# Optimization experiments

Measured on AMD Instinct MI355X. Metric: run time of the kernel, lower is better.

The kernel has to match this reference:

```python
import jax, jax.numpy as jnp
import numpy as np

N, E, IN_F, EDGE_F, HID, S = 200000, 600000, 28, 4, 128, 20000
NUM_LAYERS = 4
L = NUM_LAYERS - 1
BN_EPS = 1e-5


def setup_inputs() -> dict:
    key = jax.random.key(0)
    ks = jax.random.split(key, 20)
    p = lambda k, shape: (jax.random.normal(k, shape, dtype=jnp.float32) * 0.1)
    return {
        'x': jax.random.normal(ks[0], (N, IN_F), dtype=jnp.float32),
        'edge_index': jax.random.randint(ks[1], (2, E), 0, N),
        'edge_attr': jax.random.normal(ks[2], (E, EDGE_F), dtype=jnp.float32),
        'edge_weight': jax.random.uniform(ks[3], (E,), dtype=jnp.float32),
        'node_mask': (jax.random.uniform(ks[4], (N,)) > 0.5).astype(jnp.float32),
        'subgraphs2nodes': jax.random.randint(ks[5], (N,), 0, S),
        # layer-1 params (in_features -> hidden)
        'be1_W1': p(ks[6], (EDGE_F, IN_F)), 'be1_b1': jnp.zeros((IN_F,), jnp.float32),
        'be1_W2': p(ks[7], (IN_F, IN_F)), 'be1_b2': jnp.zeros((IN_F,), jnp.float32),
        'm1_W1': p(ks[8], (IN_F, HID)), 'm1_b1': jnp.zeros((HID,), jnp.float32),
        'm1_W2': p(ks[9], (HID, HID)), 'm1_b2': jnp.zeros((HID,), jnp.float32),
        'bn1_g': jnp.ones((HID,), jnp.float32), 'bn1_b': jnp.zeros((HID,), jnp.float32),
        'eps1': jnp.zeros((), jnp.float32),
        # layers 2..NUM_LAYERS, stacked (hidden -> hidden)
        'beW1': p(ks[10], (L, EDGE_F, HID)), 'beb1': jnp.zeros((L, HID), jnp.float32),
        'beW2': p(ks[11], (L, HID, HID)), 'beb2': jnp.zeros((L, HID), jnp.float32),
        'mW1': p(ks[12], (L, HID, HID)), 'mb1': jnp.zeros((L, HID), jnp.float32),
        'mW2': p(ks[13], (L, HID, HID)), 'mb2': jnp.zeros((L, HID), jnp.float32),
        'bng': jnp.ones((L, HID), jnp.float32), 'bnb': jnp.zeros((L, HID), jnp.float32),
        'eps': jnp.zeros((L,), jnp.float32),
    }


def _mlp2(h, W1, b1, W2, b2):
    # Linear -> ReLU -> Linear
    return jnp.dot(jax.nn.relu(jnp.dot(h, W1) + b1), W2) + b2


def _gine(x, src, dst, edge_attr, edge_weight, eps,
          beW1, beb1, beW2, beb2, W1, b1, W2, b2, g, beta):
    # bond encoder on edge features
    e = _mlp2(edge_attr, beW1, beb1, beW2, beb2)            # [E, d]
    # message: relu(x_j + e_ij) * w_ij, aggregated at dst via scatter-add
    m = jax.nn.relu(x[src] + e) * edge_weight[:, None]      # [E, d]
    aggr = jax.ops.segment_sum(m, dst, num_segments=N)      # [N, d]
    h = (1.0 + eps) * x + aggr
    # node MLP: Linear,ReLU,Linear,BN(train mode),ReLU
    h = _mlp2(h, W1, b1, W2, b2)
    mu = jnp.mean(h, axis=0)
    var = jnp.mean((h - mu) ** 2, axis=0)
    h = (h - mu) * jax.lax.rsqrt(var + BN_EPS) * g + beta
    return jax.nn.relu(h)


def reference(x, edge_index, edge_attr, edge_weight, node_mask, subgraphs2nodes,
              be1_W1, be1_b1, be1_W2, be1_b2, m1_W1, m1_b1, m1_W2, m1_b2,
              bn1_g, bn1_b, eps1,
              beW1, beb1, beW2, beb2, mW1, mb1, mW2, mb2, bng, bnb, eps):
    src, dst = edge_index[0], edge_index[1]
    h = _gine(x, src, dst, edge_attr, edge_weight, eps1,
              be1_W1, be1_b1, be1_W2, be1_b2,
              m1_W1, m1_b1, m1_W2, m1_b2, bn1_g, bn1_b)
    for i in range(L):
        h_new = _gine(h, src, dst, edge_attr, edge_weight, eps[i],
                      beW1[i], beb1[i], beW2[i], beb2[i],
                      mW1[i], mb1[i], mW2[i], mb2[i], bng[i], bnb[i])
        h = h + h_new  # residual
    # float node_mask branch + global_add_pool over subgraphs2nodes
    h = h * node_mask[:, None]
    return jax.ops.segment_sum(h, subgraphs2nodes, num_segments=S)  # [S, HID]
```

## Files before the change

kernel.cpp:

```cpp
#include <hip/hip_runtime.h>
#include <hip/hip_bf16.h>


#define BNEPS 1e-5f
#define LDA 136
#define SCAN_NB 240

typedef __attribute__((ext_vector_type(8))) short bf16x8;
typedef __attribute__((ext_vector_type(8))) unsigned short u16x8;
typedef __attribute__((ext_vector_type(4))) float f32x4;

__device__ inline short f2bf(float f) {
    __hip_bfloat16 h = __float2bfloat16(f);
    return *reinterpret_cast<short*>(&h);
}
__device__ inline unsigned short f2bfu(float f) {
    __hip_bfloat16 h = __float2bfloat16(f);
    return *reinterpret_cast<unsigned short*>(&h);
}
__device__ inline float bf2f(unsigned short u) {
    union { unsigned int i; float f; } v; v.i = ((unsigned int)u) << 16; return v.f;
}


__global__ __launch_bounds__(256) void k_prep(
    const float* __restrict__ m1W2, const float* __restrict__ beW2,
    const float* __restrict__ mW1, const float* __restrict__ mW2,
    const float* __restrict__ m1W1, const float* __restrict__ be1W2,
    short* __restrict__ out, short* __restrict__ out1, short* __restrict__ out28)
{
    __shared__ float tileS[64][65];
    int b = blockIdx.x;
    if (b == 40) {
        for (int i = threadIdx.x; i < 4096; i += 256) {
            int j = i & 7, sub = (i >> 3) & 63, nt = i >> 9;
            int quad = sub >> 4, l15 = sub & 15;
            int n = nt * 16 + l15, k = quad * 8 + j;
            out1[i] = (k < 28) ? f2bf(m1W1[(size_t)k * 128 + n]) : (short)0;
        }
        return;
    }
    if (b == 41) {
        for (int i = threadIdx.x; i < 1024; i += 256) {
            int j = i & 7, lane = (i >> 3) & 63, nt = i >> 9;
            int quad = lane >> 4, l15 = lane & 15;
            int n = nt * 16 + l15, k = quad * 8 + j;
            out28[i] = (n < 28 && k < 28) ? f2bf(be1W2[(size_t)k * 28 + n]) : (short)0;
        }
        return;
    }
    int mat = b >> 2, t = b & 3;
    const float* Wsrc;
    if (mat == 0) Wsrc = m1W2;
    else {
        int l = (mat - 1) / 3, which = (mat - 1) % 3;
        Wsrc = (which == 0) ? beW2 + (size_t)l * 16384
             : (which == 1) ? mW1 + (size_t)l * 16384
             :                mW2 + (size_t)l * 16384;
    }
    short* dst = out + (size_t)mat * 16384;
    int tr = (t >> 1) * 64, tc = (t & 1) * 64;
    for (int i = threadIdx.x; i < 4096; i += 256) {
        int r = i >> 6, c = i & 63;
        tileS[r][c] = Wsrc[(size_t)(tr + r) * 128 + (tc + c)];
    }
    __syncthreads();
    for (int i = threadIdx.x; i < 4096; i += 256) {
        int kl = i & 63, nl = i >> 6;
        int n = tc + nl, k = tr + kl;
        int fo = (((n >> 4) * 4 + (k >> 5)) * 64 + (((k >> 3) & 3) * 16 + (n & 15))) * 8 + (k & 7);
        dst[fo] = f2bf(tileS[kl][nl]);
    }
}

__global__ __launch_bounds__(256) void k_prepx(
    const float* __restrict__ x, unsigned short* __restrict__ xbf, int N)
{
    int total = N * 32;
    for (int i = blockIdx.x * 256 + threadIdx.x; i < total; i += gridDim.x * 256) {
        int n = i >> 5, c = i & 31;
        xbf[i] = (c < 28) ? f2bfu(x[(size_t)n * 28 + c]) : (unsigned short)0;
    }
}

__global__ __launch_bounds__(256) void k_count(
    const int* __restrict__ ei, int* __restrict__ counts, int E)
{
    for (int e = blockIdx.x * 256 + threadIdx.x; e < E; e += gridDim.x * 256)
        atomicAdd(&counts[ei[E + e]], 1);
}

__global__ __launch_bounds__(256) void k_count2(
    const int* __restrict__ s2n, const float* __restrict__ mask,
    int* __restrict__ counts2, int N)
{
    for (int n = blockIdx.x * 256 + threadIdx.x; n < N; n += gridDim.x * 256)
        if (mask[n] != 0.f) atomicAdd(&counts2[s2n[n]], 1);
}

__global__ __launch_bounds__(256) void k_scanA(
    const int* __restrict__ counts, int* __restrict__ bsum, int N, int seg)
{
    __shared__ int red[256];
    int b = blockIdx.x;
    int lo = b * seg, hi = min(lo + seg, N);
    int s = 0;
    for (int i = lo + threadIdx.x; i < hi; i += 256) s += counts[i];
    red[threadIdx.x] = s;
    __syncthreads();
    for (int d = 128; d > 0; d >>= 1) {
        if (threadIdx.x < d) red[threadIdx.x] += red[threadIdx.x + d];
        __syncthreads();
    }
    if (threadIdx.x == 0) bsum[b] = red[0];
}

__global__ __launch_bounds__(256) void k_scanB(
    int* __restrict__ bsum, int nb, int* __restrict__ offs, int N)
{
    __shared__ int sh[256];
    int v = (threadIdx.x < nb) ? bsum[threadIdx.x] : 0;
    sh[threadIdx.x] = v;
    __syncthreads();
    for (int d = 1; d < 256; d <<= 1) {
        int t = (threadIdx.x >= d) ? sh[threadIdx.x - d] : 0;
        __syncthreads();
        sh[threadIdx.x] += t;
        __syncthreads();
    }
    if (threadIdx.x < nb) bsum[threadIdx.x] = sh[threadIdx.x] - v;
    if (threadIdx.x == 0) offs[N] = sh[255];
}

__global__ __launch_bounds__(256) void k_scanC(
    const int* __restrict__ counts, const int* __restrict__ bsum,
    int* __restrict__ offs, int* __restrict__ cursor, int N, int seg)
{
    __shared__ int sh[256];
    int b = blockIdx.x;
    int lo = b * seg, hi = min(lo + seg, N);
    int base = bsum[b];
    for (int t0 = lo; t0 < hi; t0 += 256) {
        int i = t0 + threadIdx.x;
        int v = (i < hi) ? counts[i] : 0;
        sh[threadIdx.x] = v;
        __syncthreads();
        for (int d = 1; d < 256; d <<= 1) {
            int t = (threadIdx.x >= d) ? sh[threadIdx.x - d] : 0;
            __syncthreads();
            sh[threadIdx.x] += t;
            __syncthreads();
        }
        int excl = base + sh[threadIdx.x] - v;
        if (i < hi) { offs[i] = excl; cursor[i] = excl; }
        int tileTotal = sh[255];
        __syncthreads();
        base += tileTotal;
    }
}

__global__ __launch_bounds__(256) void k_scatter(
    const int* __restrict__ ei, const float* __restrict__ ew,
    const float4* __restrict__ ea4,
    int* __restrict__ cursor, int2* __restrict__ pmeta,
    float4* __restrict__ pea4, int E)
{
    for (int e = blockIdx.x * 256 + threadIdx.x; e < E; e += gridDim.x * 256) {
        int d = ei[E + e];
        int pos = atomicAdd(&cursor[d], 1);
        pmeta[pos] = make_int2(ei[e], __float_as_int(ew[e]));
        pea4[pos] = ea4[e];
    }
}

__global__ __launch_bounds__(256) void k_scatter2(
    const int* __restrict__ s2n, const float* __restrict__ mask,
    int* __restrict__ cursor2, int* __restrict__ perm2, int N)
{
    for (int n = blockIdx.x * 256 + threadIdx.x; n < N; n += gridDim.x * 256)
        if (mask[n] != 0.f) {
            int pos = atomicAdd(&cursor2[s2n[n]], 1);
            perm2[pos] = n;
        }
}

__global__ __launch_bounds__(256, 3) void k_emsg(
    const float4* __restrict__ pea4,
    const float* __restrict__ W1, const float* __restrict__ b1,
    const short* __restrict__ W2f, const float* __restrict__ b2,
    unsigned short* __restrict__ emsg, const int* __restrict__ offs,
    int n0, int n1)
{
    __shared__ short As[64 * LDA];
    __shared__ short Bs[16384];
    int e0 = offs[n0], e1 = offs[n1];
    int tid = threadIdx.x;
    int w = tid >> 6, lane = tid & 63;
    int l15 = lane & 15, quad = lane >> 4;
    int rb = w * 16;
    for (int i = tid; i < 2048; i += 256)
        *(bf16x8*)&Bs[i * 8] = *(const bf16x8*)&W2f[i * 8];
    int c2 = lane * 2;
    float w1a[4], w1b[4];
    #pragma unroll
    for (int a = 0; a < 4; ++a) { w1a[a] = W1[a * 128 + c2]; w1b[a] = W1[a * 128 + c2 + 1]; }
    float b1a = b1[c2], b1b = b1[c2 + 1];
    float b2r[8];
    #pragma unroll
    for (int nt = 0; nt < 8; ++nt) b2r[nt] = b2[nt * 16 + l15];
    __syncthreads();

    const float* peaf = (const float*)pea4;
    int numTiles = (e1 - e0 + 63) >> 6;
    for (int tile = blockIdx.x; tile < numTiles; tile += gridDim.x) {
        int base = e0 + tile * 64;
        int eidx = base + rb + (lane >> 2);
        float v = (eidx < e1) ? peaf[(size_t)(base + rb) * 4 + lane] : 0.f;
        #pragma unroll
        for (int e = 0; e < 16; ++e) {
            float a0v = __shfl(v, e * 4 + 0);
            float a1v = __shfl(v, e * 4 + 1);
            float a2v = __shfl(v, e * 4 + 2);
            float a3v = __shfl(v, e * 4 + 3);
            float t0 = fmaf(a0v, w1a[0], fmaf(a1v, w1a[1], fmaf(a2v, w1a[2], fmaf(a3v, w1a[3], b1a))));
            float t1 = fmaf(a0v, w1b[0], fmaf(a1v, w1b[1], fmaf(a2v, w1b[2], fmaf(a3v, w1b[3], b1b))));
            unsigned int pk = ((unsigned int)f2bfu(fmaxf(t1, 0.f)) << 16) | f2bfu(fmaxf(t0, 0.f));
            *(unsigned int*)&As[(rb + e) * LDA + c2] = pk;
        }
        f32x4 acc[8];
        #pragma unroll
        for (int nt = 0; nt < 8; ++nt) acc[nt] = (f32x4){0.f, 0.f, 0.f, 0.f};
        #pragma unroll
        for (int kt = 0; kt < 4; ++kt) {
            bf16x8 af = *(bf16x8*)&As[(rb + l15) * LDA + kt * 32 + quad * 8];
            #pragma unroll
            for (int nt = 0; nt < 8; ++nt) {
                bf16x8 bf = *(const bf16x8*)&Bs[((nt * 4 + kt) * 64 + lane) * 8];
                acc[nt] = __builtin_amdgcn_mfma_f32_16x16x32_bf16(af, bf, acc[nt], 0, 0, 0);
            }
        }
        #pragma unroll
        for (int nt = 0; nt < 8; ++nt) {
            #pragma unroll
            for (int r = 0; r < 4; ++r)
                As[(rb + quad * 4 + r) * LDA + nt * 16 + l15] = f2bf(acc[nt][r] + b2r[nt]);
        }
        #pragma unroll
        for (int it = 0; it < 4; ++it) {
            int arow = rb + it * 4 + quad;
            int gr = base + arow;
            if (gr < e1)
                *(bf16x8*)&emsg[(size_t)(gr - e0) * 128 + l15 * 8] = *(bf16x8*)&As[arow * LDA + l15 * 8];
        }
    }
}

__global__ __launch_bounds__(256, 4) void k_emsg28_mm(
    const float4* __restrict__ pea4,
    const float* __restrict__ W1, const float* __restrict__ b1,
    const short* __restrict__ W2f28,
    const float* __restrict__ b2,
    unsigned short* __restrict__ emsg28, int E)
{
    __shared__ short As[64 * 40];
    int tid = threadIdx.x;
    int w = tid >> 6, lane = tid & 63;
    int l15 = lane & 15, quad = lane >> 4;
    int rb = w * 16;
    bf16x8 B0 = *(const bf16x8*)&W2f28[(size_t)lane * 8];
    bf16x8 B1 = *(const bf16x8*)&W2f28[(size_t)(64 + lane) * 8];
    int c2 = l15 * 2;
    bool act = (c2 < 28);
    float w1a[4], w1b[4], b1a, b1b;
    #pragma unroll
    for (int a = 0; a < 4; ++a) {
        w1a[a] = act ? W1[a * 28 + c2] : 0.f;
        w1b[a] = act ? W1[a * 28 + c2 + 1] : 0.f;
    }
    b1a = act ? b1[c2] : 0.f;
    b1b = act ? b1[c2 + 1] : 0.f;
    float b2r0 = b2[l15];
    float b2r1 = (l15 < 12) ? b2[16 + l15] : 0.f;

    const float* peaf = (const float*)pea4;
    int numTiles = (E + 63) >> 6;
    for (int tile = blockIdx.x; tile < numTiles; tile += gridDim.x) {
        int base = tile * 64;
        int eidx = base + rb + (lane >> 2);
        float v = (eidx < E) ? peaf[(size_t)(base + rb) * 4 + lane] : 0.f;
        #pragma unroll
        for (int e = 0; e < 16; ++e) {
            float a0v = __shfl(v, e * 4 + 0);
            float a1v = __shfl(v, e * 4 + 1);
            float a2v = __shfl(v, e * 4 + 2);
            float a3v = __shfl(v, e * 4 + 3);
            float t0 = fmaf(a0v, w1a[0], fmaf(a1v, w1a[1], fmaf(a2v, w1a[2], fmaf(a3v, w1a[3], b1a))));
            float t1 = fmaf(a0v, w1b[0], fmaf(a1v, w1b[1], fmaf(a2v, w1b[2], fmaf(a3v, w1b[3], b1b))));
            unsigned int pk = ((unsigned int)f2bfu(fmaxf(t1, 0.f)) << 16) | f2bfu(fmaxf(t0, 0.f));
            if (quad == (e & 3))
                *(unsigned int*)&As[(rb + e) * 40 + c2] = pk;
        }
        f32x4 acc0 = (f32x4){0.f, 0.f, 0.f, 0.f};
        f32x4 acc1 = (f32x4){0.f, 0.f, 0.f, 0.f};
        bf16x8 af = *(bf16x8*)&As[(rb + l15) * 40 + quad * 8];
        acc0 = __builtin_amdgcn_mfma_f32_16x16x32_bf16(af, B0, acc0, 0, 0, 0);
        acc1 = __builtin_amdgcn_mfma_f32_16x16x32_bf16(af, B1, acc1, 0, 0, 0);
        #pragma unroll
        for (int r = 0; r < 4; ++r) {
            As[(rb + quad * 4 + r) * 40 + l15] = f2bf(acc0[r] + b2r0);
            As[(rb + quad * 4 + r) * 40 + 16 + l15] = f2bf(acc1[r] + b2r1);
        }
        #pragma unroll
        for (int it = 0; it < 4; ++it) {
            int arow = rb + it * 4 + quad;
            int gr = base + arow;
            if (gr < E && l15 < 14)
                *(ushort2*)&emsg28[(size_t)gr * 28 + c2] = *(ushort2*)&As[arow * 40 + c2];
        }
    }
}

__global__ __launch_bounds__(256) void k_gather(
    const unsigned short* __restrict__ h, const int* __restrict__ offs,
    const int2* __restrict__ pmeta, const unsigned short* __restrict__ emsg,
    unsigned short* __restrict__ a0,
    const float* __restrict__ epsp, int epsIdx,
    int n0, int n1)
{
    int grp = threadIdx.x >> 5, lane = threadIdx.x & 31;
    int n = n0 + blockIdx.x * 8 + grp;
    if (n >= n1) return;
    int e0 = offs[n0];
    int k0 = offs[n], k1 = offs[n + 1];
    float s = 1.0f + epsp[epsIdx];
    ushort4 hv0 = *(const ushort4*)&h[(size_t)n * 128 + lane * 4];
    float m0 = s * bf2f(hv0.x), m1 = s * bf2f(hv0.y);
    float m2 = s * bf2f(hv0.z), m3 = s * bf2f(hv0.w);
    int2 mtA, mtB;
    ushort4 evA, hvA, evB, hvB;
    if (k0 < k1) {
        mtA = pmeta[k0];
        evA = *(const ushort4*)&emsg[(size_t)(k0 - e0) * 128 + lane * 4];
        hvA = *(const ushort4*)&h[(size_t)mtA.x * 128 + lane * 4];
    }
    if (k0 + 1 < k1) {
        mtB = pmeta[k0 + 1];
        evB = *(const ushort4*)&emsg[(size_t)(k0 + 1 - e0) * 128 + lane * 4];
        hvB = *(const ushort4*)&h[(size_t)mtB.x * 128 + lane * 4];
    }
    for (int k = k0; k < k1; ++k) {
        float w = __int_as_float(mtA.y);
        m0 += fmaxf(bf2f(hvA.x) + bf2f(evA.x), 0.f) * w;
        m1 += fmaxf(bf2f(hvA.y) + bf2f(evA.y), 0.f) * w;
        m2 += fmaxf(bf2f(hvA.z) + bf2f(evA.z), 0.f) * w;
        m3 += fmaxf(bf2f(hvA.w) + bf2f(evA.w), 0.f) * w;
        mtA = mtB; evA = evB; hvA = hvB;
        if (k + 2 < k1) {
            mtB = pmeta[k + 2];
            evB = *(const ushort4*)&emsg[(size_t)(k + 2 - e0) * 128 + lane * 4];
            hvB = *(const ushort4*)&h[(size_t)mtB.x * 128 + lane * 4];
        }
    }
    ushort4 o;
    o.x = f2bfu(m0); o.y = f2bfu(m1); o.z = f2bfu(m2); o.w = f2bfu(m3);
    *(ushort4*)&a0[(size_t)n * 128 + lane * 4] = o;
}

__global__ __launch_bounds__(256) void k_gather28(
    const float* __restrict__ x, const unsigned short* __restrict__ xbf,
    const int* __restrict__ offs,
    const int2* __restrict__ pmeta, const unsigned short* __restrict__ emsg28,
    const float* __restrict__ eps1, float* __restrict__ u28, int N)
{
    int grp = threadIdx.x >> 5, lane = threadIdx.x & 31;
    int n = blockIdx.x * 8 + grp;
    if (n >= N || lane >= 28) return;
    float s = 1.0f + eps1[0];
    int k0 = offs[n], k1 = offs[n + 1];
    float m = 0.f;
    int2 mtA, mtB;
    unsigned short eA = 0, xA = 0, eB = 0, xB = 0;
    if (k0 < k1) {
        mtA = pmeta[k0];
        eA = emsg28[(size_t)k0 * 28 + lane];
        xA = xbf[(size_t)mtA.x * 32 + lane];
    }
    if (k0 + 1 < k1) {
        mtB = pmeta[k0 + 1];
        eB = emsg28[(size_t)(k0 + 1) * 28 + lane];
        xB = xbf[(size_t)mtB.x * 32 + lane];
    }
    for (int k = k0; k < k1; ++k) {
        float w = __int_as_float(mtA.y);
        m += fmaxf(bf2f(xA) + bf2f(eA), 0.f) * w;
        mtA = mtB; eA = eB; xA = xB;
        if (k + 2 < k1) {
            mtB = pmeta[k + 2];
            eB = emsg28[(size_t)(k + 2) * 28 + lane];
            xB = xbf[(size_t)mtB.x * 32 + lane];
        }
    }
    u28[(size_t)n * 28 + lane] = fmaf(s, x[(size_t)n * 28 + lane], m);
}

__global__ __launch_bounds__(512, 2) void k_mlp(
    const unsigned short* __restrict__ src, const short* __restrict__ W1f,
    const float* __restrict__ b1, const short* __restrict__ W2f,
    const float* __restrict__ b2, unsigned short* __restrict__ dst,
    float* __restrict__ stats, int N)
{
    __shared__ short As[256 * LDA];
    __shared__ short Bs1[16384];
    __shared__ short Bs2[16384];
    __shared__ float sstat[256];
    int tid = threadIdx.x;
    for (int i = tid; i < 2048; i += 512) {
        *(bf16x8*)&Bs1[i * 8] = *(const bf16x8*)&W1f[i * 8];
        *(bf16x8*)&Bs2[i * 8] = *(const bf16x8*)&W2f[i * 8];
    }
    if (tid < 256) sstat[tid] = 0.f;
    int w = tid >> 6, lane = tid & 63;
    int l15 = lane & 15, quad = lane >> 4;
    int rb = w * 32;
    float b1r[8], b2r[8], lsum[8], lsq[8];
    #pragma unroll
    for (int nt = 0; nt < 8; ++nt) {
        b1r[nt] = b1[nt * 16 + l15]; b2r[nt] = b2[nt * 16 + l15];
        lsum[nt] = 0.f; lsq[nt] = 0.f;
    }
    int numTiles = (N + 255) >> 8;
    bf16x8 st[8];
    {
        int tile = blockIdx.x;
        if (tile < numTiles) {
            int base = tile * 256;
            #pragma unroll
            for (int kk = 0; kk < 8; ++kk) {
                int i = tid + kk * 512;
                int rr = base + (i >> 4);
                st[kk] = (rr < N) ? *(const bf16x8*)&src[(size_t)rr * 128 + (i & 15) * 8]
                                  : (bf16x8){0, 0, 0, 0, 0, 0, 0, 0};
            }
        }
    }
    __syncthreads();

    for (int tile = blockIdx.x; tile < numTiles; tile += gridDim.x) {
        int base = tile * 256;
        #pragma unroll
        for (int kk = 0; kk < 8; ++kk) {
            int i = tid + kk * 512;
            *(bf16x8*)&As[(i >> 4) * LDA + (i & 15) * 8] = st[kk];
        }
        int tnext = tile + gridDim.x;
        if (tnext < numTiles) {
            int bn = tnext * 256;
            #pragma unroll
            for (int kk = 0; kk < 8; ++kk) {
                int i = tid + kk * 512;
                int rr = bn + (i >> 4);
                st[kk] = (rr < N) ? *(const bf16x8*)&src[(size_t)rr * 128 + (i & 15) * 8]
                                  : (bf16x8){0, 0, 0, 0, 0, 0, 0, 0};
            }
        }
        __syncthreads();
        f32x4 acc[2][8];
        #pragma unroll
        for (int rg = 0; rg < 2; ++rg)
            #pragma unroll
            for (int nt = 0; nt < 8; ++nt) acc[rg][nt] = (f32x4){0.f, 0.f, 0.f, 0.f};
        #pragma unroll
        for (int kt = 0; kt < 4; ++kt) {
            bf16x8 af0 = *(bf16x8*)&As[(rb + l15) * LDA + kt * 32 + quad * 8];
            bf16x8 af1 = *(bf16x8*)&As[(rb + 16 + l15) * LDA + kt * 32 + quad * 8];
            #pragma unroll
            for (int nt = 0; nt < 8; ++nt) {
                bf16x8 bf = *(const bf16x8*)&Bs1[((nt * 4 + kt) * 64 + lane) * 8];
                acc[0][nt] = __builtin_amdgcn_mfma_f32_16x16x32_bf16(af0, bf, acc[0][nt], 0, 0, 0);
                acc[1][nt] = __builtin_amdgcn_mfma_f32_16x16x32_bf16(af1, bf, acc[1][nt], 0, 0, 0);
            }
        }
        #pragma unroll
        for (int rg = 0; rg < 2; ++rg)
            #pragma unroll
            for (int nt = 0; nt < 8; ++nt)
                #pragma unroll
                for (int r = 0; r < 4; ++r)
                    As[(rb + rg * 16 + quad * 4 + r) * LDA + nt * 16 + l15] =
                        f2bf(fmaxf(acc[rg][nt][r] + b1r[nt], 0.f));
        #pragma unroll
        for (int rg = 0; rg < 2; ++rg)
            #pragma unroll
            for (int nt = 0; nt < 8; ++nt) acc[rg][nt] = (f32x4){0.f, 0.f, 0.f, 0.f};
        #pragma unroll
        for (int kt = 0; kt < 4; ++kt) {
            bf16x8 af0 = *(bf16x8*)&As[(rb + l15) * LDA + kt * 32 + quad * 8];
            bf16x8 af1 = *(bf16x8*)&As[(rb + 16 + l15) * LDA + kt * 32 + quad * 8];
            #pragma unroll
            for (int nt = 0; nt < 8; ++nt) {
                bf16x8 bf = *(const bf16x8*)&Bs2[((nt * 4 + kt) * 64 + lane) * 8];
                acc[0][nt] = __builtin_amdgcn_mfma_f32_16x16x32_bf16(af0, bf, acc[0][nt], 0, 0, 0);
                acc[1][nt] = __builtin_amdgcn_mfma_f32_16x16x32_bf16(af1, bf, acc[1][nt], 0, 0, 0);
            }
        }
        #pragma unroll
        for (int rg = 0; rg < 2; ++rg)
            #pragma unroll
            for (int nt = 0; nt < 8; ++nt) {
                int row0 = base + rb + rg * 16 + quad * 4;
                #pragma unroll
                for (int r = 0; r < 4; ++r) {
                    float z = acc[rg][nt][r] + b2r[nt];
                    if (row0 + r < N) { lsum[nt] += z; lsq[nt] = fmaf(z, z, lsq[nt]); }
                    As[(rb + rg * 16 + quad * 4 + r) * LDA + nt * 16 + l15] = f2bf(z);
                }
            }
        #pragma unroll
        for (int it = 0; it < 8; ++it) {
            int arow = rb + it * 4 + quad;
            int rr = base + arow;
            if (rr < N)
                *(bf16x8*)&dst[(size_t)rr * 128 + l15 * 8] = *(bf16x8*)&As[arow * LDA + l15 * 8];
        }
        __syncthreads();
    }
    #pragma unroll
    for (int nt = 0; nt < 8; ++nt) {
        atomicAdd(&sstat[nt * 16 + l15], lsum[nt]);
        atomicAdd(&sstat[128 + nt * 16 + l15], lsq[nt]);
    }
    __syncthreads();
    if (tid < 256) atomicAdd(&stats[tid], sstat[tid]);
}

__global__ __launch_bounds__(512, 2) void k_mlp1(
    const float* __restrict__ u28, const short* __restrict__ W1f,
    const float* __restrict__ b1, const short* __restrict__ W2f,
    const float* __restrict__ b2, unsigned short* __restrict__ dst,
    float* __restrict__ stats, int N)
{
    __shared__ short A28[256 * 40];
    __shared__ short As[256 * LDA];
    __shared__ short Bs1[4096];
    __shared__ short Bs2[16384];
    __shared__ float sstat[256];
    int tid = threadIdx.x;
    if (tid < 512) {
        int i = tid;
        *(bf16x8*)&Bs1[i * 8] = *(const bf16x8*)&W1f[i * 8];
    }
    for (int i = tid; i < 2048; i += 512)
        *(bf16x8*)&Bs2[i * 8] = *(const bf16x8*)&W2f[i * 8];
    for (int i = tid; i < 1024; i += 512) {
        int row = i >> 2, c = 28 + (i & 3);
        A28[row * 40 + c] = 0;
    }
    if (tid < 256) sstat[tid] = 0.f;
    int w = tid >> 6, lane = tid & 63;
    int l15 = lane & 15, quad = lane >> 4;
    int rb = w * 32;
    float b1r[8], b2r[8], lsum[8], lsq[8];
    #pragma unroll
    for (int nt = 0; nt < 8; ++nt) {
        b1r[nt] = b1[nt * 16 + l15]; b2r[nt] = b2[nt * 16 + l15];
        lsum[nt] = 0.f; lsq[nt] = 0.f;
    }
    int numTiles = (N + 255) >> 8;
    float stf[14];
    {
        int tile = blockIdx.x;
        if (tile < numTiles) {
            int base = tile * 256;
            #pragma unroll
            for (int kk = 0; kk < 14; ++kk) {
                int idx = tid + kk * 512;
                int row = idx / 28, col = idx - row * 28;
                int rr = base + row;
                stf[kk] = (rr < N) ? u28[(size_t)rr * 28 + col] : 0.f;
            }
        }
    }
    __syncthreads();

    for (int tile = blockIdx.x; tile < numTiles; tile += gridDim.x) {
        int base = tile * 256;
        #pragma unroll
        for (int kk = 0; kk < 14; ++kk) {
            int idx = tid + kk * 512;
            int row = idx / 28, col = idx - row * 28;
            A28[row * 40 + col] = f2bf(stf[kk]);
        }
        int tnext = tile + gridDim.x;
        if (tnext < numTiles) {
            int bn = tnext * 256;
            #pragma unroll
            for (int kk = 0; kk < 14; ++kk) {
                int idx = tid + kk * 512;
                int row = idx / 28, col = idx - row * 28;
                int rr = bn + row;
                stf[kk] = (rr < N) ? u28[(size_t)rr * 28 + col] : 0.f;
            }
        }
        __syncthreads();
        f32x4 acc[2][8];
        #pragma unroll
        for (int rg = 0; rg < 2; ++rg)
            #pragma unroll
            for (int nt = 0; nt < 8; ++nt) acc[rg][nt] = (f32x4){0.f, 0.f, 0.f, 0.f};
        {
            bf16x8 af0 = *(bf16x8*)&A28[(rb + l15) * 40 + quad * 8];
            bf16x8 af1 = *(bf16x8*)&A28[(rb + 16 + l15) * 40 + quad * 8];
            #pragma unroll
            for (int nt = 0; nt < 8; ++nt) {
                bf16x8 bf = *(const bf16x8*)&Bs1[(nt * 64 + lane) * 8];
                acc[0][nt] = __builtin_amdgcn_mfma_f32_16x16x32_bf16(af0, bf, acc[0][nt], 0, 0, 0);
                acc[1][nt] = __builtin_amdgcn_mfma_f32_16x16x32_bf16(af1, bf, acc[1][nt], 0, 0, 0);
            }
        }
        #pragma unroll
        for (int rg = 0; rg < 2; ++rg)
            #pragma unroll
            for (int nt = 0; nt < 8; ++nt)
                #pragma unroll
                for (int r = 0; r < 4; ++r)
                    As[(rb + rg * 16 + quad * 4 + r) * LDA + nt * 16 + l15] =
                        f2bf(fmaxf(acc[rg][nt][r] + b1r[nt], 0.f));
        #pragma unroll
        for (int rg = 0; rg < 2; ++rg)
            #pragma unroll
            for (int nt = 0; nt < 8; ++nt) acc[rg][nt] = (f32x4){0.f, 0.f, 0.f, 0.f};
        #pragma unroll
        for (int kt = 0; kt < 4; ++kt) {
            bf16x8 af0 = *(bf16x8*)&As[(rb + l15) * LDA + kt * 32 + quad * 8];
            bf16x8 af1 = *(bf16x8*)&As[(rb + 16 + l15) * LDA + kt * 32 + quad * 8];
            #pragma unroll
            for (int nt = 0; nt < 8; ++nt) {
                bf16x8 bf = *(const bf16x8*)&Bs2[((nt * 4 + kt) * 64 + lane) * 8];
                acc[0][nt] = __builtin_amdgcn_mfma_f32_16x16x32_bf16(af0, bf, acc[0][nt], 0, 0, 0);
                acc[1][nt] = __builtin_amdgcn_mfma_f32_16x16x32_bf16(af1, bf, acc[1][nt], 0, 0, 0);
            }
        }
        #pragma unroll
        for (int rg = 0; rg < 2; ++rg)
            #pragma unroll
            for (int nt = 0; nt < 8; ++nt) {
                int row0 = base + rb + rg * 16 + quad * 4;
                #pragma unroll
                for (int r = 0; r < 4; ++r) {
                    float z = acc[rg][nt][r] + b2r[nt];
                    if (row0 + r < N) { lsum[nt] += z; lsq[nt] = fmaf(z, z, lsq[nt]); }
                    As[(rb + rg * 16 + quad * 4 + r) * LDA + nt * 16 + l15] = f2bf(z);
                }
            }
        #pragma unroll
        for (int it = 0; it < 8; ++it) {
            int arow = rb + it * 4 + quad;
            int rr = base + arow;
            if (rr < N)
                *(bf16x8*)&dst[(size_t)rr * 128 + l15 * 8] = *(bf16x8*)&As[arow * LDA + l15 * 8];
        }
        __syncthreads();
    }
    #pragma unroll
    for (int nt = 0; nt < 8; ++nt) {
        atomicAdd(&sstat[nt * 16 + l15], lsum[nt]);
        atomicAdd(&sstat[128 + nt * 16 + l15], lsq[nt]);
    }
    __syncthreads();
    if (tid < 256) atomicAdd(&stats[tid], sstat[tid]);
}

__global__ __launch_bounds__(128) void k_stats(
    const float* __restrict__ stats, const float* __restrict__ g,
    const float* __restrict__ b, float* __restrict__ ss, float invN)
{
    int j = threadIdx.x;
    float mu  = stats[j] * invN;
    float var = fmaf(stats[128 + j], invN, -mu * mu);
    float sc  = rsqrtf(fmaxf(var, 0.f) + BNEPS) * g[j];
    ss[j] = sc;
    ss[128 + j] = fmaf(-mu, sc, b[j]);
}

__global__ __launch_bounds__(256) void k_bn(
    const unsigned short* __restrict__ z, const float* __restrict__ ss,
    unsigned short* __restrict__ h, int residual, int N)
{
    int idx8 = blockIdx.x * 256 + threadIdx.x;
    int stride = gridDim.x * 256;
    int c0 = (idx8 & 15) * 8;
    float scl[8], sht[8];
    #pragma unroll
    for (int r = 0; r < 8; ++r) { scl[r] = ss[c0 + r]; sht[r] = ss[128 + c0 + r]; }
    int total8 = N * 16;
    for (; idx8 < total8; idx8 += stride) {
        int n = idx8 >> 4;
        u16x8 z8 = *(const u16x8*)&z[(size_t)n * 128 + c0];
        float hn[8];
        #pragma unroll
        for (int r = 0; r < 8; ++r)
            hn[r] = fmaxf(fmaf(bf2f(z8[r]), scl[r], sht[r]), 0.f);
        if (residual) {
            u16x8 h8 = *(const u16x8*)&h[(size_t)n * 128 + c0];
            #pragma unroll
            for (int r = 0; r < 8; ++r) hn[r] += bf2f(h8[r]);
        }
        u16x8 o;
        #pragma unroll
        for (int r = 0; r < 8; ++r) o[r] = f2bfu(hn[r]);
        *(u16x8*)&h[(size_t)n * 128 + c0] = o;
    }
}

__global__ __launch_bounds__(256) void k_poolbn(
    const unsigned short* __restrict__ z, const unsigned short* __restrict__ hprev,
    const float* __restrict__ ss, const int* __restrict__ offs2,
    const int* __restrict__ perm2, float* __restrict__ out, int S)
{
    int w = threadIdx.x >> 6, lane = threadIdx.x & 63;
    int s = blockIdx.x * 4 + w;
    if (s >= S) return;
    int c0 = lane * 2;
    float scl0 = ss[c0], scl1 = ss[c0 + 1];
    float sht0 = ss[128 + c0], sht1 = ss[128 + c0 + 1];
    int k0 = offs2[s], k1 = offs2[s + 1];
    float a0 = 0.f, a1 = 0.f;
    for (int k = k0; k < k1; ++k) {
        int n = perm2[k];
        ushort2 zv = *(const ushort2*)&z[(size_t)n * 128 + c0];
        ushort2 hv = *(const ushort2*)&hprev[(size_t)n * 128 + c0];
        a0 += fmaxf(fmaf(bf2f(zv.x), scl0, sht0), 0.f) + bf2f(hv.x);
        a1 += fmaxf(fmaf(bf2f(zv.y), scl1, sht1), 0.f) + bf2f(hv.y);
    }
    *(float2*)&out[(size_t)s * 128 + c0] = make_float2(a0, a1);
}

extern "C" void kernel_launch(void* const* d_in, const int* in_sizes, int n_in,
                              void* d_out, int out_size, void* d_ws, size_t ws_size,
                              hipStream_t stream) {
    const float* x    = (const float*)d_in[0];
    const int*   ei   = (const int*)d_in[1];
    const float* ea   = (const float*)d_in[2];
    const float* ew   = (const float*)d_in[3];
    const float* mask = (const float*)d_in[4];
    const int*   s2n  = (const int*)d_in[5];
    const float* be1W1 = (const float*)d_in[6];
    const float* be1b1 = (const float*)d_in[7];
    const float* be1W2 = (const float*)d_in[8];
    const float* be1b2 = (const float*)d_in[9];
    const float* m1W1  = (const float*)d_in[10];
    const float* m1b1  = (const float*)d_in[11];
    const float* m1W2  = (const float*)d_in[12];
    const float* m1b2  = (const float*)d_in[13];
    const float* bn1g  = (const float*)d_in[14];
    const float* bn1b  = (const float*)d_in[15];
    const float* eps1  = (const float*)d_in[16];
    const float* beW1  = (const float*)d_in[17];
    const float* beb1  = (const float*)d_in[18];
    const float* beW2  = (const float*)d_in[19];
    const float* beb2  = (const float*)d_in[20];
    const float* mW1   = (const float*)d_in[21];
    const float* mb1   = (const float*)d_in[22];
    const float* mW2   = (const float*)d_in[23];
    const float* mb2   = (const float*)d_in[24];
    const float* bng   = (const float*)d_in[25];
    const float* bnb   = (const float*)d_in[26];
    const float* epsL  = (const float*)d_in[27];

    const int N = in_sizes[0] / 28;
    const int E = in_sizes[1] / 2;
    const int S = out_size / 128;
    const float invN = 1.0f / (float)N;
    const int NS = N / 2;
    const int EMC = E / 2 + 8192;

    auto al16 = [](size_t v) { return (v + 15) & ~(size_t)15; };
    char* ws = (char*)d_ws;
    size_t offH      = 0;
    size_t offA0     = al16(offH + (size_t)N * 256);
    size_t offEm     = al16(offA0 + (size_t)N * 256);
    size_t emBytes   = (size_t)EMC * 256;
    if ((size_t)E * 56 > emBytes) emBytes = (size_t)E * 56;
    size_t offStats  = al16(offEm + emBytes);
    size_t offSS     = al16(offStats + 4096);
    size_t offWts    = al16(offSS + 1024);
    size_t offCounts = al16(offWts + 10 * 16384 * 2 + 4096 * 2 + 1024 * 2);
    size_t offOffs   = al16(offCounts + (size_t)N * 4);
    size_t offCursor = al16(offOffs + (size_t)(N + 1) * 4);
    size_t offPmeta  = al16(offCursor + (size_t)N * 4);
    size_t offPea    = al16(offPmeta + (size_t)E * 8);
    size_t offBsum   = al16(offPea + (size_t)E * 16);
    size_t offCnt2   = al16(offBsum + SCAN_NB * 4);
    size_t offOffs2  = al16(offCnt2 + (size_t)S * 4);
    size_t offCur2   = al16(offOffs2 + (size_t)(S + 1) * 4);
    size_t offPerm2  = al16(offCur2 + (size_t)S * 4);
    size_t need      = offPerm2 + (size_t)N * 4;
    if (ws_size < need) return;

    unsigned short* h    = (unsigned short*)(ws + offH);
    unsigned short* a0   = (unsigned short*)(ws + offA0);
    unsigned short* emsg = (unsigned short*)(ws + offEm);
    float* u28    = (float*)(ws + offA0);
    unsigned short* xbf = (unsigned short*)(ws + offA0 + 26214400);
    float* stats  = (float*)(ws + offStats);
    float* ssbuf  = (float*)(ws + offSS);
    short* wts    = (short*)(ws + offWts);
    short* w1p    = wts + 10 * 16384;
    short* w2p28  = w1p + 4096;
    int*   counts = (int*)(ws + offCounts);
    int*   offs   = (int*)(ws + offOffs);
    int*   cursor = (int*)(ws + offCursor);
    int2*  pmeta  = (int2*)(ws + offPmeta);
    float4* pea4  = (float4*)(ws + offPea);
    int*   bsum   = (int*)(ws + offBsum);
    int*   cnt2   = (int*)(ws + offCnt2);
    int*   offs2  = (int*)(ws + offOffs2);
    int*   cur2   = (int*)(ws + offCur2);
    int*   perm2  = (int*)(ws + offPerm2);
    const float4* ea4 = (const float4*)ea;

    hipMemsetAsync(stats, 0, 4 * 256 * sizeof(float), stream);
    hipMemsetAsync(counts, 0, (size_t)N * sizeof(int), stream);
    hipMemsetAsync(cnt2, 0, (size_t)S * sizeof(int), stream);

    k_prep<<<42, 256, 0, stream>>>(m1W2, beW2, mW1, mW2, m1W1, be1W2, wts, w1p, w2p28);
    k_prepx<<<512, 256, 0, stream>>>(x, xbf, N);

    const int seg = (N + SCAN_NB - 1) / SCAN_NB;
    k_count<<<1024, 256, 0, stream>>>(ei, counts, E);
    k_scanA<<<SCAN_NB, 256, 0, stream>>>(counts, bsum, N, seg);
    k_scanB<<<1, 256, 0, stream>>>(bsum, SCAN_NB, offs, N);
    k_scanC<<<SCAN_NB, 256, 0, stream>>>(counts, bsum, offs, cursor, N, seg);
    k_scatter<<<1024, 256, 0, stream>>>(ei, ew, ea4, cursor, pmeta, pea4, E);

    const int seg2 = (S + SCAN_NB - 1) / SCAN_NB;
    k_count2<<<512, 256, 0, stream>>>(s2n, mask, cnt2, N);
    k_scanA<<<SCAN_NB, 256, 0, stream>>>(cnt2, bsum, S, seg2);
    k_scanB<<<1, 256, 0, stream>>>(bsum, SCAN_NB, offs2, S);
    k_scanC<<<SCAN_NB, 256, 0, stream>>>(cnt2, bsum, offs2, cur2, S, seg2);
    k_scatter2<<<512, 256, 0, stream>>>(s2n, mask, cur2, perm2, N);

    auto wt_be = [&](int l) { return wts + (size_t)(1 + 3 * l + 0) * 16384; };
    auto wt_m1 = [&](int l) { return wts + (size_t)(1 + 3 * l + 1) * 16384; };
    auto wt_m2 = [&](int l) { return wts + (size_t)(1 + 3 * l + 2) * 16384; };

    k_emsg28_mm<<<2048, 256, 0, stream>>>(pea4, be1W1, be1b1, w2p28, be1b2, emsg, E);
    k_gather28<<<(N + 7) / 8, 256, 0, stream>>>(x, xbf, offs, pmeta, emsg, eps1, u28, N);
    k_mlp1<<<256, 512, 0, stream>>>(u28, w1p, m1b1, wts , m1b2, h, stats, N);
    k_stats<<<1, 128, 0, stream>>>(stats, bn1g, bn1b, ssbuf, invN);
    k_bn<<<2048, 256, 0, stream>>>(h, ssbuf, h, 0, N);

    for (int l = 0; l < 3; ++l) {
        for (int c = 0; c < 2; ++c) {
            int n0 = (c == 0) ? 0 : NS;
            int n1 = (c == 0) ? NS : N;
            k_emsg<<<2048, 256, 0, stream>>>(pea4,
                beW1 + (size_t)l * 512, beb1 + (size_t)l * 128,
                wt_be(l), beb2 + (size_t)l * 128, emsg, offs, n0, n1);
            k_gather<<<(n1 - n0 + 7) / 8, 256, 0, stream>>>(h, offs, pmeta, emsg, a0,
                epsL, l, n0, n1);
        }
        k_mlp<<<256, 512, 0, stream>>>(a0, wt_m1(l), mb1 + (size_t)l * 128,
                                       wt_m2(l), mb2 + (size_t)l * 128, a0,
                                       stats + 256 * (l + 1), N);
        k_stats<<<1, 128, 0, stream>>>(stats + 256 * (l + 1),
            bng + (size_t)l * 128, bnb + (size_t)l * 128, ssbuf, invN);
        if (l < 2) {
            k_bn<<<2048, 256, 0, stream>>>(a0, ssbuf, h, 1, N);
        }
    }

    k_poolbn<<<(S + 3) / 4, 256, 0, stream>>>(a0, h, ssbuf, offs2, perm2,
                                              (float*)d_out, S);
}
```

Measured before the change: 1.035 ms.

## Make MLP kernels wave-independent with direct global A loads and 1024-thread blocks

Restructures k_mlp and k_mlp1 so each wave handles its own 16-row slice. Input fragments are loaded straight from global memory into MFMA registers instead of being staged through a shared 256-row tile. Per-tile block-wide __syncthreads and the register prefetch of the next tile are removed, and blocks grow to 1024 threads to keep more waves resident. The trade-off is the loss of explicit load prefetching and a tighter register budget under launch_bounds(1024,4), which risks spilling; the A fragment loads are also less coalesced.

New measurement: 1.056 ms. 1.02x slower.

```diff
diff --git a/kernel.cpp b/kernel.cpp
--- a/kernel.cpp
+++ b/kernel.cpp
@@ -403,126 +403,86 @@
     u28[(size_t)n * 28 + lane] = fmaf(s, x[(size_t)n * 28 + lane], m);
 }
 
-__global__ __launch_bounds__(512, 2) void k_mlp(
+__global__ __launch_bounds__(1024, 4) void k_mlp(
     const unsigned short* __restrict__ src, const short* __restrict__ W1f,
     const float* __restrict__ b1, const short* __restrict__ W2f,
     const float* __restrict__ b2, unsigned short* __restrict__ dst,
     float* __restrict__ stats, int N)
 {
-    __shared__ short As[256 * LDA];
     __shared__ short Bs1[16384];
     __shared__ short Bs2[16384];
+    __shared__ short As[16 * 16 * LDA];
     __shared__ float sstat[256];
     int tid = threadIdx.x;
-    for (int i = tid; i < 2048; i += 512) {
+    for (int i = tid; i < 2048; i += 1024) {
         *(bf16x8*)&Bs1[i * 8] = *(const bf16x8*)&W1f[i * 8];
         *(bf16x8*)&Bs2[i * 8] = *(const bf16x8*)&W2f[i * 8];
     }
     if (tid < 256) sstat[tid] = 0.f;
     int w = tid >> 6, lane = tid & 63;
     int l15 = lane & 15, quad = lane >> 4;
-    int rb = w * 32;
+    short* myAs = &As[w * 16 * LDA];
     float b1r[8], b2r[8], lsum[8], lsq[8];
     #pragma unroll
     for (int nt = 0; nt < 8; ++nt) {
         b1r[nt] = b1[nt * 16 + l15]; b2r[nt] = b2[nt * 16 + l15];
         lsum[nt] = 0.f; lsq[nt] = 0.f;
     }
+    __syncthreads();
+
     int numTiles = (N + 255) >> 8;
-    bf16x8 st[8];
-    {
-        int tile = blockIdx.x;
-        if (tile < numTiles) {
-            int base = tile * 256;
-            #pragma unroll
-            for (int kk = 0; kk < 8; ++kk) {
-                int i = tid + kk * 512;
-                int rr = base + (i >> 4);
-                st[kk] = (rr < N) ? *(const bf16x8*)&src[(size_t)rr * 128 + (i & 15) * 8]
-                                  : (bf16x8){0, 0, 0, 0, 0, 0, 0, 0};
-            }
-        }
-    }
-    __syncthreads();
-
     for (int tile = blockIdx.x; tile < numTiles; tile += gridDim.x) {
-        int base = tile * 256;
-        #pragma unroll
-        for (int kk = 0; kk < 8; ++kk) {
-            int i = tid + kk * 512;
-            *(bf16x8*)&As[(i >> 4) * LDA + (i & 15) * 8] = st[kk];
-        }
-        int tnext = tile + gridDim.x;
-        if (tnext < numTiles) {
-            int bn = tnext * 256;
-            #pragma unroll
-            for (int kk = 0; kk < 8; ++kk) {
-                int i = tid + kk * 512;
-                int rr = bn + (i >> 4);
-                st[kk] = (rr < N) ? *(const bf16x8*)&src[(size_t)rr * 128 + (i & 15) * 8]
-                                  : (bf16x8){0, 0, 0, 0, 0, 0, 0, 0};
-            }
-        }
-        __syncthreads();
-        f32x4 acc[2][8];
-        #pragma unroll
-        for (int rg = 0; rg < 2; ++rg)
-            #pragma unroll
-            for (int nt = 0; nt < 8; ++nt) acc[rg][nt] = (f32x4){0.f, 0.f, 0.f, 0.f};
+        int rowbase = tile * 256 + w * 16;
+        int arow = rowbase + l15;
+        const unsigned short* srow = src + (size_t)arow * 128;
+        f32x4 acc[8];
+        #pragma unroll
+        for (int nt = 0; nt < 8; ++nt) acc[nt] = (f32x4){0.f, 0.f, 0.f, 0.f};
         #pragma unroll
         for (int kt = 0; kt < 4; ++kt) {
-            bf16x8 af0 = *(bf16x8*)&As[(rb + l15) * LDA + kt * 32 + quad * 8];
-            bf16x8 af1 = *(bf16x8*)&As[(rb + 16 + l15) * LDA + kt * 32 + quad * 8];
+            bf16x8 af = (arow < N) ? *(const bf16x8*)&srow[kt * 32 + quad * 8]
+                                   : (bf16x8){0, 0, 0, 0, 0, 0, 0, 0};
             #pragma unroll
             for (int nt = 0; nt < 8; ++nt) {
                 bf16x8 bf = *(const bf16x8*)&Bs1[((nt * 4 + kt) * 64 + lane) * 8];
-                acc[0][nt] = __builtin_amdgcn_mfma_f32_16x16x32_bf16(af0, bf, acc[0][nt], 0, 0, 0);
-                acc[1][nt] = __builtin_amdgcn_mfma_f32_16x16x32_bf16(af1, bf, acc[1][nt], 0, 0, 0);
+                acc[nt] = __builtin_amdgcn_mfma_f32_16x16x32_bf16(af, bf, acc[nt], 0, 0, 0);
             }
         }
         #pragma unroll
-        for (int rg = 0; rg < 2; ++rg)
-            #pragma unroll
-            for (int nt = 0; nt < 8; ++nt)
-                #pragma unroll
-                for (int r = 0; r < 4; ++r)
-                    As[(rb + rg * 16 + quad * 4 + r) * LDA + nt * 16 + l15] =
-                        f2bf(fmaxf(acc[rg][nt][r] + b1r[nt], 0.f));
-        #pragma unroll
-        for (int rg = 0; rg < 2; ++rg)
-            #pragma unroll
-            for (int nt = 0; nt < 8; ++nt) acc[rg][nt] = (f32x4){0.f, 0.f, 0.f, 0.f};
+        for (int nt = 0; nt < 8; ++nt)
+            #pragma unroll
+            for (int r = 0; r < 4; ++r)
+                myAs[(quad * 4 + r) * LDA + nt * 16 + l15] =
+                    f2bf(fmaxf(acc[nt][r] + b1r[nt], 0.f));
+        #pragma unroll
+        for (int nt = 0; nt < 8; ++nt) acc[nt] = (f32x4){0.f, 0.f, 0.f, 0.f};
         #pragma unroll
         for (int kt = 0; kt < 4; ++kt) {
-            bf16x8 af0 = *(bf16x8*)&As[(rb + l15) * LDA + kt * 32 + quad * 8];
-            bf16x8 af1 = *(bf16x8*)&As[(rb + 16 + l15) * LDA + kt * 32 + quad * 8];
+            bf16x8 af = *(bf16x8*)&myAs[l15 * LDA + kt * 32 + quad * 8];
             #pragma unroll
             for (int nt = 0; nt < 8; ++nt) {
                 bf16x8 bf = *(const bf16x8*)&Bs2[((nt * 4 + kt) * 64 + lane) * 8];
-                acc[0][nt] = __builtin_amdgcn_mfma_f32_16x16x32_bf16(af0, bf, acc[0][nt], 0, 0, 0);
-                acc[1][nt] = __builtin_amdgcn_mfma_f32_16x16x32_bf16(af1, bf, acc[1][nt], 0, 0, 0);
+                acc[nt] = __builtin_amdgcn_mfma_f32_16x16x32_bf16(af, bf, acc[nt], 0, 0, 0);
             }
         }
         #pragma unroll
-        for (int rg = 0; rg < 2; ++rg)
-            #pragma unroll
-            for (int nt = 0; nt < 8; ++nt) {
-                int row0 = base + rb + rg * 16 + quad * 4;
-                #pragma unroll
-                for (int r = 0; r < 4; ++r) {
-                    float z = acc[rg][nt][r] + b2r[nt];
-                    if (row0 + r < N) { lsum[nt] += z; lsq[nt] = fmaf(z, z, lsq[nt]); }
-                    As[(rb + rg * 16 + quad * 4 + r) * LDA + nt * 16 + l15] = f2bf(z);
-                }
+        for (int nt = 0; nt < 8; ++nt) {
+            int row0 = rowbase + quad * 4;
+            #pragma unroll
+            for (int r = 0; r < 4; ++r) {
+                float z = acc[nt][r] + b2r[nt];
+                if (row0 + r < N) { lsum[nt] += z; lsq[nt] = fmaf(z, z, lsq[nt]); }
+                myAs[(quad * 4 + r) * LDA + nt * 16 + l15] = f2bf(z);
             }
-        #pragma unroll
-        for (int it = 0; it < 8; ++it) {
-            int arow = rb + it * 4 + quad;
-            int rr = base + arow;
+        }
+        #pragma unroll
+        for (int s = 0; s < 4; ++s) {
+            int i = lane + s * 64;
+            int lrow = i >> 4, c8 = i & 15;
+            int rr = rowbase + lrow;
             if (rr < N)
-                *(bf16x8*)&dst[(size_t)rr * 128 + l15 * 8] = *(bf16x8*)&As[arow * LDA + l15 * 8];
-        }
-        __syncthreads();
+                *(bf16x8*)&dst[(size_t)rr * 128 + c8 * 8] = *(bf16x8*)&myAs[lrow * LDA + c8 * 8];
+        }
     }
     #pragma unroll
     for (int nt = 0; nt < 8; ++nt) {
@@ -533,133 +493,90 @@
     if (tid < 256) atomicAdd(&stats[tid], sstat[tid]);
 }
 
-__global__ __launch_bounds__(512, 2) void k_mlp1(
+__global__ __launch_bounds__(1024, 4) void k_mlp1(
     const float* __restrict__ u28, const short* __restrict__ W1f,
     const float* __restrict__ b1, const short* __restrict__ W2f,
     const float* __restrict__ b2, unsigned short* __restrict__ dst,
     float* __restrict__ stats, int N)
 {
-    __shared__ short A28[256 * 40];
-    __shared__ short As[256 * LDA];
     __shared__ short Bs1[4096];
     __shared__ short Bs2[16384];
+    __shared__ short As[16 * 16 * LDA];
     __shared__ float sstat[256];
     int tid = threadIdx.x;
-    if (tid < 512) {
-        int i = tid;
-        *(bf16x8*)&Bs1[i * 8] = *(const bf16x8*)&W1f[i * 8];
-    }
-    for (int i = tid; i < 2048; i += 512)
+    if (tid < 512)
+        *(bf16x8*)&Bs1[tid * 8] = *(const bf16x8*)&W1f[tid * 8];
+    for (int i = tid; i < 2048; i += 1024)
         *(bf16x8*)&Bs2[i * 8] = *(const bf16x8*)&W2f[i * 8];
-    for (int i = tid; i < 1024; i += 512) {
-        int row = i >> 2, c = 28 + (i & 3);
-        A28[row * 40 + c] = 0;
-    }
     if (tid < 256) sstat[tid] = 0.f;
     int w = tid >> 6, lane = tid & 63;
     int l15 = lane & 15, quad = lane >> 4;
-    int rb = w * 32;
+    short* myAs = &As[w * 16 * LDA];
     float b1r[8], b2r[8], lsum[8], lsq[8];
     #pragma unroll
     for (int nt = 0; nt < 8; ++nt) {
         b1r[nt] = b1[nt * 16 + l15]; b2r[nt] = b2[nt * 16 + l15];
         lsum[nt] = 0.f; lsq[nt] = 0.f;
     }
+    __syncthreads();
+
     int numTiles = (N + 255) >> 8;
-    float stf[14];
-    {
-        int tile = blockIdx.x;
-        if (tile < numTiles) {
-            int base = tile * 256;
-            #pragma unroll
-            for (int kk = 0; kk < 14; ++kk) {
-                int idx = tid + kk * 512;
-                int row = idx / 28, col = idx - row * 28;
-                int rr = base + row;
-                stf[kk] = (rr < N) ? u28[(size_t)rr * 28 + col] : 0.f;
-            }
-        }
-    }
-    __syncthreads();
-
     for (int tile = blockIdx.x; tile < numTiles; tile += gridDim.x) {
-        int base = tile * 256;
-        #pragma unroll
-        for (int kk = 0; kk < 14; ++kk) {
-            int idx = tid + kk * 512;
-            int row = idx / 28, col = idx - row * 28;
-            A28[row * 40 + col] = f2bf(stf[kk]);
-        }
-        int tnext = tile + gridDim.x;
-        if (tnext < numTiles) {
-            int bn = tnext * 256;
-            #pragma unroll
-            for (int kk = 0; kk < 14; ++kk) {
-                int idx = tid + kk * 512;
-                int row = idx / 28, col = idx - row * 28;
-                int rr = bn + row;
-                stf[kk] = (rr < N) ? u28[(size_t)rr * 28 + col] : 0.f;
-            }
-        }
-        __syncthreads();
-        f32x4 acc[2][8];
-        #pragma unroll
-        for (int rg = 0; rg < 2; ++rg)
-            #pragma unroll
-            for (int nt = 0; nt < 8; ++nt) acc[rg][nt] = (f32x4){0.f, 0.f, 0.f, 0.f};
-        {
-            bf16x8 af0 = *(bf16x8*)&A28[(rb + l15) * 40 + quad * 8];
-            bf16x8 af1 = *(bf16x8*)&A28[(rb + 16 + l15) * 40 + quad * 8];
-            #pragma unroll
-            for (int nt = 0; nt < 8; ++nt) {
-                bf16x8 bf = *(const bf16x8*)&Bs1[(nt * 64 + lane) * 8];
-                acc[0][nt] = __builtin_amdgcn_mfma_f32_16x16x32_bf16(af0, bf, acc[0][nt], 0, 0, 0);
-                acc[1][nt] = __builtin_amdgcn_mfma_f32_16x16x32_bf16(af1, bf, acc[1][nt], 0, 0, 0);
-            }
-        }
-        #pragma unroll
-        for (int rg = 0; rg < 2; ++rg)
-            #pragma unroll
-            for (int nt = 0; nt < 8; ++nt)
-                #pragma unroll
-                for (int r = 0; r < 4; ++r)
-                    As[(rb + rg * 16 + quad * 4 + r) * LDA + nt * 16 + l15] =
-                        f2bf(fmaxf(acc[rg][nt][r] + b1r[nt], 0.f));
-        #pragma unroll
-        for (int rg = 0; rg < 2; ++rg)
-            #pragma unroll
-            for (int nt = 0; nt < 8; ++nt) acc[rg][nt] = (f32x4){0.f, 0.f, 0.f, 0.f};
+        int rowbase = tile * 256 + w * 16;
+        int arow = rowbase + l15;
+        const float* urow = u28 + (size_t)arow * 28;
+        float4 fa = make_float4(0.f, 0.f, 0.f, 0.f);
+        float4 fb = make_float4(0.f, 0.f, 0.f, 0.f);
+        if (arow < N) {
+            fa = *(const float4*)&urow[quad * 8];
+            if (quad < 3) fb = *(const float4*)&urow[quad * 8 + 4];
+        }
+        bf16x8 af1;
+        af1[0] = f2bf(fa.x); af1[1] = f2bf(fa.y); af1[2] = f2bf(fa.z); af1[3] = f2bf(fa.w);
+        af1[4] = f2bf(fb.x); af1[5] = f2bf(fb.y); af1[6] = f2bf(fb.z); af1[7] = f2bf(fb.w);
+        f32x4 acc[8];
+        #pragma unroll
+        for (int nt = 0; nt < 8; ++nt) acc[nt] = (f32x4){0.f, 0.f, 0.f, 0.f};
+        #pragma unroll
+        for (int nt = 0; nt < 8; ++nt) {
+            bf16x8 bf = *(const bf16x8*)&Bs1[(nt * 64 + lane) * 8];
+            acc[nt] = __builtin_amdgcn_mfma_f32_16x16x32_bf16(af1, bf, acc[nt], 0, 0, 0);
+        }
+        #pragma unroll
+        for (int nt = 0; nt < 8; ++nt)
+            #pragma unroll
+            for (int r = 0; r < 4; ++r)
+                myAs[(quad * 4 + r) * LDA + nt * 16 + l15] =
+                    f2bf(fmaxf(acc[nt][r] + b1r[nt], 0.f));
+        #pragma unroll
+        for (int nt = 0; nt < 8; ++nt) acc[nt] = (f32x4){0.f, 0.f, 0.f, 0.f};
         #pragma unroll
         for (int kt = 0; kt < 4; ++kt) {
-            bf16x8 af0 = *(bf16x8*)&As[(rb + l15) * LDA + kt * 32 + quad * 8];
-            bf16x8 af1 = *(bf16x8*)&As[(rb + 16 + l15) * LDA + kt * 32 + quad * 8];
+            bf16x8 af = *(bf16x8*)&myAs[l15 * LDA + kt * 32 + quad * 8];
             #pragma unroll
             for (int nt = 0; nt < 8; ++nt) {
                 bf16x8 bf = *(const bf16x8*)&Bs2[((nt * 4 + kt) * 64 + lane) * 8];
-                acc[0][nt] = __builtin_amdgcn_mfma_f32_16x16x32_bf16(af0, bf, acc[0][nt], 0, 0, 0);
-                acc[1][nt] = __builtin_amdgcn_mfma_f32_16x16x32_bf16(af1, bf, acc[1][nt], 0, 0, 0);
+                acc[nt] = __builtin_amdgcn_mfma_f32_16x16x32_bf16(af, bf, acc[nt], 0, 0, 0);
             }
         }
         #pragma unroll
-        for (int rg = 0; rg < 2; ++rg)
-            #pragma unroll
-            for (int nt = 0; nt < 8; ++nt) {
-                int row0 = base + rb + rg * 16 + quad * 4;
-                #pragma unroll
-                for (int r = 0; r < 4; ++r) {
-                    float z = acc[rg][nt][r] + b2r[nt];
-                    if (row0 + r < N) { lsum[nt] += z; lsq[nt] = fmaf(z, z, lsq[nt]); }
-                    As[(rb + rg * 16 + quad * 4 + r) * LDA + nt * 16 + l15] = f2bf(z);
-                }
+        for (int nt = 0; nt < 8; ++nt) {
+            int row0 = rowbase + quad * 4;
+            #pragma unroll
+            for (int r = 0; r < 4; ++r) {
+                float z = acc[nt][r] + b2r[nt];
+                if (row0 + r < N) { lsum[nt] += z; lsq[nt] = fmaf(z, z, lsq[nt]); }
+                myAs[(quad * 4 + r) * LDA + nt * 16 + l15] = f2bf(z);
             }
-        #pragma unroll
-        for (int it = 0; it < 8; ++it) {
-            int arow = rb + it * 4 + quad;
-            int rr = base + arow;
+        }
+        #pragma unroll
+        for (int s = 0; s < 4; ++s) {
+            int i = lane + s * 64;
+            int lrow = i >> 4, c8 = i & 15;
+            int rr = rowbase + lrow;
             if (rr < N)
-                *(bf16x8*)&dst[(size_t)rr * 128 + l15 * 8] = *(bf16x8*)&As[arow * LDA + l15 * 8];
-        }
-        __syncthreads();
+                *(bf16x8*)&dst[(size_t)rr * 128 + c8 * 8] = *(bf16x8*)&myAs[lrow * LDA + c8 * 8];
+        }
     }
     #pragma unroll
     for (int nt = 0; nt < 8; ++nt) {
@@ -846,7 +763,7 @@
 
     k_emsg28_mm<<<2048, 256, 0, stream>>>(pea4, be1W1, be1b1, w2p28, be1b2, emsg, E);
     k_gather28<<<(N + 7) / 8, 256, 0, stream>>>(x, xbf, offs, pmeta, emsg, eps1, u28, N);
-    k_mlp1<<<256, 512, 0, stream>>>(u28, w1p, m1b1, wts , m1b2, h, stats, N);
+    k_mlp1<<<256, 1024, 0, stream>>>(u28, w1p, m1b1, wts , m1b2, h, stats, N);
     k_stats<<<1, 128, 0, stream>>>(stats, bn1g, bn1b, ssbuf, invN);
     k_bn<<<2048, 256, 0, stream>>>(h, ssbuf, h, 0, N);
 
@@ -860,9 +777,9 @@
             k_gather<<<(n1 - n0 + 7) / 8, 256, 0, stream>>>(h, offs, pmeta, emsg, a0,
                 epsL, l, n0, n1);
         }
-        k_mlp<<<256, 512, 0, stream>>>(a0, wt_m1(l), mb1 + (size_t)l * 128,
-                                       wt_m2(l), mb2 + (size_t)l * 128, a0,
-                                       stats + 256 * (l + 1), N);
+        k_mlp<<<256, 1024, 0, stream>>>(a0, wt_m1(l), mb1 + (size_t)l * 128,
+                                        wt_m2(l), mb2 + (size_t)l * 128, a0,
+                                        stats + 256 * (l + 1), N);
         k_stats<<<1, 128, 0, stream>>>(stats + 256 * (l + 1),
             bng + (size_t)l * 128, bnb + (size_t)l * 128, ssbuf, invN);
         if (l < 2) {
```
